# Optimization experiments

Measured on AMD Instinct MI355X. Metric: run time of the kernel, lower is better.

The kernel has to match this reference:

```python
import jax, jax.numpy as jnp
import numpy as np
import math

B, N_SEQ, SEQ_LEN, C_M = 1, 256, 256, 256
N_HEADS, C_HIDDEN = 8, 32
HC = N_HEADS * C_HIDDEN
LN_EPS = 1e-5


def setup_inputs() -> dict:
    key = jax.random.key(0)
    ks = jax.random.split(key, 8)
    s_in = 1.0 / math.sqrt(C_M)
    s_out = 1.0 / math.sqrt(HC)
    return {
        "m": jax.random.normal(ks[0], (B, N_SEQ, SEQ_LEN, C_M), dtype=jnp.float32),
        "ln_w": jnp.ones((C_M,), dtype=jnp.float32),
        "ln_b": jnp.zeros((C_M,), dtype=jnp.float32),
        "wq": jax.random.normal(ks[1], (C_M, HC), dtype=jnp.float32) * s_in,
        "wk": jax.random.normal(ks[2], (C_M, HC), dtype=jnp.float32) * s_in,
        "wv": jax.random.normal(ks[3], (C_M, HC), dtype=jnp.float32) * s_in,
        "wg": jax.random.normal(ks[4], (C_M, HC), dtype=jnp.float32) * s_in,
        "bg": jnp.zeros((HC,), dtype=jnp.float32),
        "wo": jax.random.normal(ks[5], (HC, C_M), dtype=jnp.float32) * s_out,
        "bo": jnp.zeros((C_M,), dtype=jnp.float32),
    }


def reference(m, ln_w, ln_b, wq, wk, wv, wg, bg, wo, bo):
    b, s, l, _ = m.shape  # [B, n_seq, seq_len, c_m]
    # LayerNorm over c_m
    mu = jnp.mean(m, axis=-1, keepdims=True)
    var = jnp.mean(jnp.square(m - mu), axis=-1, keepdims=True)
    mn = (m - mu) * jax.lax.rsqrt(var + LN_EPS) * ln_w + ln_b  # [B, S, L, c_m]
    mt = jnp.swapaxes(mn, 1, 2)  # [B, L, S, c_m] -- attend over n_seq per column
    # QKV projections (no bias), split heads: [B, L, H, S, ch]
    def proj(w):
        return jnp.transpose(
            (mt @ w).reshape(b, l, s, N_HEADS, C_HIDDEN), (0, 1, 3, 2, 4)
        )
    q, k, v = proj(wq), proj(wk), proj(wv)
    logits = jnp.einsum("blhsc,blhtc->blhst", q, k) / math.sqrt(C_HIDDEN)
    weights = jax.nn.softmax(logits, axis=-1)
    o = jnp.einsum("blhst,blhtc->blhsc", weights, v)  # [B, L, H, S, ch]
    # Faithful to source: permute(0,2,1,3,4) -> [B, H, L, S, ch], then raw reshape
    o = jnp.transpose(o, (0, 2, 1, 3, 4))
    o = o.reshape(b, s, l, HC)  # data-scrambling reshape, as in source
    # Sigmoid gating on layer-normed input (m.transpose(1,2).transpose(1,2) == mn)
    g = jax.nn.sigmoid(mn @ wg + bg)  # [B, S, L, HC]
    o = g * o
    return o @ wo + bo  # [B, S, L, c_m]
```

## Files before the change

### kernel.cpp

```cpp
#include <hip/hip_runtime.h>

typedef unsigned short u16;
typedef __attribute__((ext_vector_type(8))) short bf16x8;
typedef __attribute__((ext_vector_type(4))) float f32x4;

__device__ __forceinline__ u16 f2b(float f){
  __bf16 h = (__bf16)f;
  return __builtin_bit_cast(u16, h);
}

__global__ __launch_bounds__(256) void k_pre(const float* __restrict__ m,
    const float* __restrict__ lw, const float* __restrict__ lb,
    const float* __restrict__ wq, const float* __restrict__ wk,
    const float* __restrict__ wv, const float* __restrict__ wg,
    const float* __restrict__ wo,
    u16* __restrict__ mnb, u16* __restrict__ mnb2, u16* __restrict__ WT){
  __shared__ u16 T[16*264];
  int bx = blockIdx.x;
  int tid = threadIdx.x;
  if (bx < 2048){
    int l = bx>>3;
    int s0 = (bx&7)*32 + (tid>>6)*8;
    int ln = tid&63;
    float4 w = *(const float4*)(lw + ln*4);
    float4 b = *(const float4*)(lb + ln*4);
    #pragma unroll
    for (int i=0;i<8;++i){
      int s = s0 + i;
      float4 x = *(const float4*)(m + ((size_t)s*256 + l)*256 + ln*4);
      float s1 = x.x+x.y+x.z+x.w;
      float s2 = x.x*x.x + x.y*x.y + x.z*x.z + x.w*x.w;
      #pragma unroll
      for (int off=32; off>0; off>>=1){
        s1 += __shfl_xor(s1, off);
        s2 += __shfl_xor(s2, off);
      }
      float mu  = s1*(1.0f/256.0f);
      float inv = rsqrtf(s2*(1.0f/256.0f) - mu*mu + 1e-5f);
      u16 o[4];
      o[0] = f2b((x.x-mu)*inv*w.x + b.x);
      o[1] = f2b((x.y-mu)*inv*w.y + b.y);
      o[2] = f2b((x.z-mu)*inv*w.z + b.z);
      o[3] = f2b((x.w-mu)*inv*w.w + b.w);
      *(ushort4*)(mnb  + ((size_t)l*256 + s)*256 + ln*4) = *(ushort4*)o;
      *(ushort4*)(mnb2 + ((size_t)s*256 + l)*256 + ln*4) = *(ushort4*)o;
    }
  } else {
    int bb = bx - 2048;
    int z = bb>>4, n0 = (bb&15)*16;
    const float* W = (z==0)?wq:(z==1)?wk:(z==2)?wv:(z==3)?wg:wo;
    int nl = tid&15;
    #pragma unroll
    for (int i=0;i<16;++i){
      int cm = i*16 + (tid>>4);
      T[nl*264 + cm] = f2b(W[(size_t)cm*256 + n0 + nl]);
    }
    __syncthreads();
    int n = tid>>4, cc = (tid&15)*16;
    uint4 a = *(const uint4*)&T[n*264 + cc];
    uint4 c = *(const uint4*)&T[n*264 + cc + 8];
    *(uint4*)&WT[(size_t)z*65536 + (size_t)(n0+n)*256 + cc]     = a;
    *(uint4*)&WT[(size_t)z*65536 + (size_t)(n0+n)*256 + cc + 8] = c;
  }
}

__global__ __launch_bounds__(256,3) void k_fused(const u16* __restrict__ mnb,
    const u16* __restrict__ mnb2, const u16* __restrict__ WT,
    const float* __restrict__ bg, const float* __restrict__ bo,
    float* __restrict__ outp){
  __shared__ u16 smem[26880];
  u16* QS = smem;
  u16* KS = smem + 10240;
  u16* VT = smem + 18432;
  u16* PB = smem;
  float* OS = (float*)smem;
  u16* GS = smem + 18432;

  int bx = blockIdx.x;
  int l = ((bx&7)<<5) | (bx>>6);
  int h = (bx>>3)&7;
  int tid = threadIdx.x;
  int lane = tid&63, wid = tid>>6, quad = lane>>4, lo = lane&15;
  int m0 = wid*64;
  f32x4 z4 = {0.f,0.f,0.f,0.f};

  const u16* Abase = mnb + (size_t)l*65536;
  const u16* Bq = WT + (size_t)h*32*256;
  const u16* Bk = WT + (size_t)65536 + (size_t)h*32*256;
  const u16* Bv = WT + (size_t)2*65536 + (size_t)h*32*256;
  f32x4 acc[4][6];
  #pragma unroll
  for (int a=0;a<4;++a)
    #pragma unroll
    for (int b=0;b<6;++b) acc[a][b]=z4;

  for (int ks=0; ks<8; ++ks){
    bf16x8 af[4];
    #pragma unroll
    for (int mt=0; mt<4; ++mt)
      af[mt] = *(const bf16x8*)(Abase + (size_t)(m0+mt*16+lo)*256 + ks*32 + quad*8);
    bf16x8 bq[2], bk2[2], bv2[2];
    #pragma unroll
    for (int c2=0; c2<2; ++c2){
      bq[c2]  = *(const bf16x8*)(Bq + (size_t)(c2*16+lo)*256 + ks*32 + quad*8);
      bk2[c2] = *(const bf16x8*)(Bk + (size_t)(c2*16+lo)*256 + ks*32 + quad*8);
      bv2[c2] = *(const bf16x8*)(Bv + (size_t)(c2*16+lo)*256 + ks*32 + quad*8);
    }
    #pragma unroll
    for (int mt=0; mt<4; ++mt){
      #pragma unroll
      for (int c2=0; c2<2; ++c2){
        acc[mt][0+c2] = __builtin_amdgcn_mfma_f32_16x16x32_bf16(af[mt], bq[c2],  acc[mt][0+c2], 0,0,0);
        acc[mt][2+c2] = __builtin_amdgcn_mfma_f32_16x16x32_bf16(af[mt], bk2[c2], acc[mt][2+c2], 0,0,0);
        acc[mt][4+c2] = __builtin_amdgcn_mfma_f32_16x16x32_bf16(af[mt], bv2[c2], acc[mt][4+c2], 0,0,0);
      }
    }
  }
  #pragma unroll
  for (int mt=0; mt<4; ++mt)
    #pragma unroll
    for (int ntl=0; ntl<2; ++ntl)
      #pragma unroll
      for (int r=0; r<4; ++r){
        int s = m0 + mt*16 + quad*4 + r;
        QS[s*40 + ntl*16+lo] = f2b(acc[mt][0+ntl][r]);
        KS[s*32 + ntl*16+lo] = f2b(acc[mt][2+ntl][r]);
        VT[(ntl*16+lo)*264 + s] = f2b(acc[mt][4+ntl][r]);
      }
  bf16x8 qf[4];
  #pragma unroll
  for (int mt=0; mt<4; ++mt)
    qf[mt] = *(const bf16x8*)&QS[(m0+mt*16+lo)*40 + quad*8];
  __syncthreads();

  const float scale = 0.17677669529663687f;
  float lr[16];
  #pragma unroll
  for (int i=0;i<16;++i) lr[i]=0.f;
  f32x4 o_acc[4][2];
  #pragma unroll
  for (int a=0;a<4;++a){ o_acc[a][0]=z4; o_acc[a][1]=z4; }
  int pbase = wid*64*40;

  for (int ts=0; ts<8; ++ts){
    bf16x8 kf[2];
    #pragma unroll
    for (int ntl=0; ntl<2; ++ntl)
      kf[ntl] = *(const bf16x8*)&KS[(ts*32+ntl*16+lo)*32 + quad*8];
    bf16x8 vf[2];
    #pragma unroll
    for (int nc=0; nc<2; ++nc)
      vf[nc] = *(const bf16x8*)&VT[(nc*16+lo)*264 + ts*32 + quad*8];
    #pragma unroll
    for (int mt=0; mt<4; ++mt){
      f32x4 sa[2];
      sa[0] = __builtin_amdgcn_mfma_f32_16x16x32_bf16(qf[mt], kf[0], z4, 0,0,0);
      sa[1] = __builtin_amdgcn_mfma_f32_16x16x32_bf16(qf[mt], kf[1], z4, 0,0,0);
      #pragma unroll
      for (int ntl=0; ntl<2; ++ntl)
        #pragma unroll
        for (int r=0; r<4; ++r){
          float p = __expf(sa[ntl][r]*scale);
          lr[mt*4+r] += p;
          PB[pbase + (mt*16+quad*4+r)*40 + ntl*16+lo] = f2b(p);
        }
      bf16x8 paf = *(const bf16x8*)&PB[pbase + (mt*16+lo)*40 + quad*8];
      o_acc[mt][0] = __builtin_amdgcn_mfma_f32_16x16x32_bf16(paf, vf[0], o_acc[mt][0], 0,0,0);
      o_acc[mt][1] = __builtin_amdgcn_mfma_f32_16x16x32_bf16(paf, vf[1], o_acc[mt][1], 0,0,0);
    }
  }
  #pragma unroll
  for (int i=0;i<16;++i){
    float v = lr[i];
    v += __shfl_xor(v, 1);
    v += __shfl_xor(v, 2);
    v += __shfl_xor(v, 4);
    v += __shfl_xor(v, 8);
    lr[i] = 1.0f / v;
  }
  __syncthreads();
  #pragma unroll
  for (int mt=0; mt<4; ++mt)
    #pragma unroll
    for (int nc=0; nc<2; ++nc)
      #pragma unroll
      for (int r=0; r<4; ++r){
        int s = m0 + mt*16 + quad*4 + r;
        int c = nc*16 + lo;
        OS[s*32 + c] = o_acc[mt][nc][r] * lr[mt*4+r];
      }
  __syncthreads();

  int sp  = h*32 + (l>>3);
  int l0p = (l&7)*32;
  int wn0 = wid*64;
  const u16* Gw = WT + (size_t)3*65536;
  const u16* A2 = mnb2 + (size_t)sp*65536;
  f32x4 gacc[2][4];
  #pragma unroll
  for (int a=0;a<2;++a)
    #pragma unroll
    for (int b=0;b<4;++b) gacc[a][b]=z4;
  for (int ks=0; ks<8; ++ks){
    bf16x8 ga[2];
    #pragma unroll
    for (int mt2=0; mt2<2; ++mt2)
      ga[mt2] = *(const bf16x8*)(A2 + (size_t)(l0p+mt2*16+lo)*256 + ks*32 + quad*8);
    bf16x8 gb[4];
    #pragma unroll
    for (int nt=0; nt<4; ++nt)
      gb[nt] = *(const bf16x8*)(Gw + (size_t)(wn0+nt*16+lo)*256 + ks*32 + quad*8);
    #pragma unroll
    for (int mt2=0; mt2<2; ++mt2)
      #pragma unroll
      for (int nt=0; nt<4; ++nt)
        gacc[mt2][nt] = __builtin_amdgcn_mfma_f32_16x16x32_bf16(ga[mt2], gb[nt], gacc[mt2][nt], 0,0,0);
  }
  #pragma unroll
  for (int nt=0; nt<4; ++nt){
    int n = wn0 + nt*16 + lo;
    float bgn = bg[n];
    #pragma unroll
    for (int mt2=0; mt2<2; ++mt2)
      #pragma unroll
      for (int r=0; r<4; ++r){
        int j = mt2*16 + quad*4 + r;
        float g = 1.f/(1.f + __expf(-(gacc[mt2][nt][r] + bgn)));
        GS[j*264 + n] = f2b(g * OS[j*256 + n]);
      }
  }
  __syncthreads();

  const u16* Ow = WT + (size_t)4*65536;
  f32x4 pacc[2][4];
  #pragma unroll
  for (int a=0;a<2;++a)
    #pragma unroll
    for (int b=0;b<4;++b) pacc[a][b]=z4;
  for (int ks=0; ks<8; ++ks){
    bf16x8 pa[2];
    #pragma unroll
    for (int mt2=0; mt2<2; ++mt2)
      pa[mt2] = *(const bf16x8*)&GS[(mt2*16+lo)*264 + ks*32 + quad*8];
    bf16x8 pb[4];
    #pragma unroll
    for (int nt=0; nt<4; ++nt)
      pb[nt] = *(const bf16x8*)(Ow + (size_t)(wn0+nt*16+lo)*256 + ks*32 + quad*8);
    #pragma unroll
    for (int mt2=0; mt2<2; ++mt2)
      #pragma unroll
      for (int nt=0; nt<4; ++nt)
        pacc[mt2][nt] = __builtin_amdgcn_mfma_f32_16x16x32_bf16(pa[mt2], pb[nt], pacc[mt2][nt], 0,0,0);
  }
  #pragma unroll
  for (int nt=0; nt<4; ++nt){
    int n = wn0 + nt*16 + lo;
    float bon = bo[n];
    #pragma unroll
    for (int mt2=0; mt2<2; ++mt2)
      #pragma unroll
      for (int r=0; r<4; ++r){
        int j = mt2*16 + quad*4 + r;
        outp[((size_t)sp*256 + l0p + j)*256 + n] = pacc[mt2][nt][r] + bon;
      }
  }
}

extern "C" void kernel_launch(void* const* d_in, const int* in_sizes, int n_in,
                              void* d_out, int out_size, void* d_ws, size_t ws_size,
                              hipStream_t stream){
  const float* m  = (const float*)d_in[0];
  const float* lw = (const float*)d_in[1];
  const float* lb = (const float*)d_in[2];
  const float* wq = (const float*)d_in[3];
  const float* wk = (const float*)d_in[4];
  const float* wv = (const float*)d_in[5];
  const float* wg = (const float*)d_in[6];
  const float* bg = (const float*)d_in[7];
  const float* wo = (const float*)d_in[8];
  const float* bo = (const float*)d_in[9];

  u16* mnb  = (u16*)d_ws;
  u16* mnb2 = mnb  + (size_t)16777216;
  u16* WT   = mnb2 + (size_t)16777216;
  float* out = (float*)d_out;

  k_pre  <<<2128, 256, 0, stream>>>(m, lw, lb, wq, wk, wv, wg, wo, mnb, mnb2, WT);
  k_fused<<<2048, 256, 0, stream>>>(mnb, mnb2, WT, bg, bo, out);
}
```

Measured before the change: 308.5 us.

## Drop second normalized copy; gather gate operand via async LDS loads

The pre-kernel no longer writes a second s-major copy of the layer-normed activations. That removes 32 MB of bf16 writes and the later reads of that copy. The fused kernel instead gathers the gate GEMM's A rows from the single l-major copy straight into LDS with global_load_lds, using an XOR swizzle, and issues this at kernel start so it overlaps the QKV projection. Q is staged through a small per-wave scratch, V is stored in a new interleaved layout, and each thread in the LN kernel now handles 8 elements. The gathered loads are strided (512 B chunks, 128 KB apart), which may hurt coalescing, and an extra barrier is added.

Result: faster. 300.4 us (-2.6%).

```diff
diff --git a/kernel.cpp b/kernel.cpp
--- a/kernel.cpp
+++ b/kernel.cpp
@@ -7,6 +7,12 @@
 __device__ __forceinline__ u16 f2b(float f){
   __bf16 h = (__bf16)f;
   return __builtin_bit_cast(u16, h);
+}
+
+__device__ __forceinline__ void gload_lds16(const void* g, void* l){
+  __builtin_amdgcn_global_load_lds(
+      (const __attribute__((address_space(1))) unsigned int*)g,
+      (__attribute__((address_space(3))) unsigned int*)l, 16, 0, 0);
 }
 
 __global__ __launch_bounds__(256) void k_pre(const float* __restrict__ m,
@@ -14,36 +20,44 @@
     const float* __restrict__ wq, const float* __restrict__ wk,
     const float* __restrict__ wv, const float* __restrict__ wg,
     const float* __restrict__ wo,
-    u16* __restrict__ mnb, u16* __restrict__ mnb2, u16* __restrict__ WT){
+    u16* __restrict__ mnb, u16* __restrict__ WT){
   __shared__ u16 T[16*264];
-  int bx = blockIdx.x;
-  int tid = threadIdx.x;
+  int bx = blockIdx.x, tid = threadIdx.x;
   if (bx < 2048){
     int l = bx>>3;
-    int s0 = (bx&7)*32 + (tid>>6)*8;
-    int ln = tid&63;
-    float4 w = *(const float4*)(lw + ln*4);
-    float4 b = *(const float4*)(lb + ln*4);
-    #pragma unroll
-    for (int i=0;i<8;++i){
-      int s = s0 + i;
-      float4 x = *(const float4*)(m + ((size_t)s*256 + l)*256 + ln*4);
-      float s1 = x.x+x.y+x.z+x.w;
-      float s2 = x.x*x.x + x.y*x.y + x.z*x.z + x.w*x.w;
-      #pragma unroll
-      for (int off=32; off>0; off>>=1){
+    int w = tid>>6, ln = tid&63, half = ln>>5, lh = ln&31;
+    float4 wa = *(const float4*)(lw + lh*8);
+    float4 wb = *(const float4*)(lw + lh*8 + 4);
+    float4 ba = *(const float4*)(lb + lh*8);
+    float4 bb = *(const float4*)(lb + lh*8 + 4);
+    #pragma unroll
+    for (int i=0;i<4;++i){
+      int s = (bx&7)*32 + w*8 + i*2 + half;
+      const float* mp = m + ((size_t)s*256 + l)*256 + lh*8;
+      float4 xa = *(const float4*)mp;
+      float4 xb = *(const float4*)(mp+4);
+      float s1 = (xa.x+xa.y)+(xa.z+xa.w) + (xb.x+xb.y)+(xb.z+xb.w);
+      float s2 = xa.x*xa.x+xa.y*xa.y+xa.z*xa.z+xa.w*xa.w
+               + xb.x*xb.x+xb.y*xb.y+xb.z*xb.z+xb.w*xb.w;
+      #pragma unroll
+      for (int off=16; off>0; off>>=1){
         s1 += __shfl_xor(s1, off);
         s2 += __shfl_xor(s2, off);
       }
       float mu  = s1*(1.0f/256.0f);
       float inv = rsqrtf(s2*(1.0f/256.0f) - mu*mu + 1e-5f);
-      u16 o[4];
-      o[0] = f2b((x.x-mu)*inv*w.x + b.x);
-      o[1] = f2b((x.y-mu)*inv*w.y + b.y);
-      o[2] = f2b((x.z-mu)*inv*w.z + b.z);
-      o[3] = f2b((x.w-mu)*inv*w.w + b.w);
-      *(ushort4*)(mnb  + ((size_t)l*256 + s)*256 + ln*4) = *(ushort4*)o;
-      *(ushort4*)(mnb2 + ((size_t)s*256 + l)*256 + ln*4) = *(ushort4*)o;
+      u16 o[8];
+      o[0]=f2b((xa.x-mu)*inv*wa.x+ba.x);
+      o[1]=f2b((xa.y-mu)*inv*wa.y+ba.y);
+      o[2]=f2b((xa.z-mu)*inv*wa.z+ba.z);
+      o[3]=f2b((xa.w-mu)*inv*wa.w+ba.w);
+      o[4]=f2b((xb.x-mu)*inv*wb.x+bb.x);
+      o[5]=f2b((xb.y-mu)*inv*wb.y+bb.y);
+      o[6]=f2b((xb.z-mu)*inv*wb.z+bb.z);
+      o[7]=f2b((xb.w-mu)*inv*wb.w+bb.w);
+      u16* op = mnb + ((size_t)l*256 + s)*256 + lh*8;
+      *(ushort4*)op     = *(ushort4*)&o[0];
+      *(ushort4*)(op+4) = *(ushort4*)&o[4];
     }
   } else {
     int bb = bx - 2048;
@@ -65,16 +79,14 @@
 }
 
 __global__ __launch_bounds__(256,3) void k_fused(const u16* __restrict__ mnb,
-    const u16* __restrict__ mnb2, const u16* __restrict__ WT,
-    const float* __restrict__ bg, const float* __restrict__ bo,
-    float* __restrict__ outp){
-  __shared__ u16 smem[26880];
-  u16* QS = smem;
-  u16* KS = smem + 10240;
-  u16* VT = smem + 18432;
-  u16* PB = smem;
+    const u16* __restrict__ WT, const float* __restrict__ bg,
+    const float* __restrict__ bo, float* __restrict__ outp){
+  __shared__ u16 smem[27136];
+  u16* KS  = smem + 2560;
+  u16* VT2 = smem + 10752;
+  u16* GAB = smem + 18944;
   float* OS = (float*)smem;
-  u16* GS = smem + 18432;
+  u16* GS  = smem + 16384;
 
   int bx = blockIdx.x;
   int l = ((bx&7)<<5) | (bx>>6);
@@ -82,7 +94,22 @@
   int tid = threadIdx.x;
   int lane = tid&63, wid = tid>>6, quad = lane>>4, lo = lane&15;
   int m0 = wid*64;
+  u16* SC = smem + wid*640;
   f32x4 z4 = {0.f,0.f,0.f,0.f};
+  int sp  = h*32 + (l>>3);
+  int l0p = (l&7)*32;
+
+  {
+    const char* mb = (const char*)mnb;
+    #pragma unroll
+    for (int c2=0;c2<4;++c2){
+      int r   = wid*8 + c2*2 + (lane>>5);
+      int dst = (wid*8 + c2*2)*256;
+      size_t src = (size_t)(l0p + r)*131072 + (size_t)sp*512
+                 + (size_t)((((lane&31)*16) ^ ((r&7)<<4)));
+      gload_lds16(mb + src, &GAB[dst]);
+    }
+  }
 
   const u16* Abase = mnb + (size_t)l*65536;
   const u16* Bq = WT + (size_t)h*32*256;
@@ -122,15 +149,21 @@
     for (int ntl=0; ntl<2; ++ntl)
       #pragma unroll
       for (int r=0; r<4; ++r){
-        int s = m0 + mt*16 + quad*4 + r;
-        QS[s*40 + ntl*16+lo] = f2b(acc[mt][0+ntl][r]);
-        KS[s*32 + ntl*16+lo] = f2b(acc[mt][2+ntl][r]);
-        VT[(ntl*16+lo)*264 + s] = f2b(acc[mt][4+ntl][r]);
+        int t = m0 + mt*16 + quad*4 + r;
+        int c = ntl*16 + lo;
+        KS[t*32 + c] = f2b(acc[mt][2+ntl][r]);
+        VT2[(t>>3)*256 + c*8 + (t&7)] = f2b(acc[mt][4+ntl][r]);
       }
   bf16x8 qf[4];
   #pragma unroll
-  for (int mt=0; mt<4; ++mt)
-    qf[mt] = *(const bf16x8*)&QS[(m0+mt*16+lo)*40 + quad*8];
+  for (int mt=0; mt<4; ++mt){
+    #pragma unroll
+    for (int ntl=0; ntl<2; ++ntl)
+      #pragma unroll
+      for (int r=0; r<4; ++r)
+        SC[(quad*4+r)*40 + ntl*16+lo] = f2b(acc[mt][0+ntl][r]);
+    qf[mt] = *(const bf16x8*)&SC[lo*40 + quad*8];
+  }
   __syncthreads();
 
   const float scale = 0.17677669529663687f;
@@ -140,7 +173,6 @@
   f32x4 o_acc[4][2];
   #pragma unroll
   for (int a=0;a<4;++a){ o_acc[a][0]=z4; o_acc[a][1]=z4; }
-  int pbase = wid*64*40;
 
   for (int ts=0; ts<8; ++ts){
     bf16x8 kf[2];
@@ -150,7 +182,7 @@
     bf16x8 vf[2];
     #pragma unroll
     for (int nc=0; nc<2; ++nc)
-      vf[nc] = *(const bf16x8*)&VT[(nc*16+lo)*264 + ts*32 + quad*8];
+      vf[nc] = *(const bf16x8*)&VT2[(ts*4+quad)*256 + (nc*16+lo)*8];
     #pragma unroll
     for (int mt=0; mt<4; ++mt){
       f32x4 sa[2];
@@ -162,9 +194,9 @@
         for (int r=0; r<4; ++r){
           float p = __expf(sa[ntl][r]*scale);
           lr[mt*4+r] += p;
-          PB[pbase + (mt*16+quad*4+r)*40 + ntl*16+lo] = f2b(p);
+          SC[(quad*4+r)*40 + ntl*16+lo] = f2b(p);
         }
-      bf16x8 paf = *(const bf16x8*)&PB[pbase + (mt*16+lo)*40 + quad*8];
+      bf16x8 paf = *(const bf16x8*)&SC[lo*40 + quad*8];
       o_acc[mt][0] = __builtin_amdgcn_mfma_f32_16x16x32_bf16(paf, vf[0], o_acc[mt][0], 0,0,0);
       o_acc[mt][1] = __builtin_amdgcn_mfma_f32_16x16x32_bf16(paf, vf[1], o_acc[mt][1], 0,0,0);
     }
@@ -191,11 +223,8 @@
       }
   __syncthreads();
 
-  int sp  = h*32 + (l>>3);
-  int l0p = (l&7)*32;
   int wn0 = wid*64;
   const u16* Gw = WT + (size_t)3*65536;
-  const u16* A2 = mnb2 + (size_t)sp*65536;
   f32x4 gacc[2][4];
   #pragma unroll
   for (int a=0;a<2;++a)
@@ -204,8 +233,10 @@
   for (int ks=0; ks<8; ++ks){
     bf16x8 ga[2];
     #pragma unroll
-    for (int mt2=0; mt2<2; ++mt2)
-      ga[mt2] = *(const bf16x8*)(A2 + (size_t)(l0p+mt2*16+lo)*256 + ks*32 + quad*8);
+    for (int mt2=0; mt2<2; ++mt2){
+      int j = mt2*16 + lo;
+      ga[mt2] = *(const bf16x8*)&GAB[j*256 + ((ks*32 + quad*8) ^ ((j&7)<<3))];
+    }
     bf16x8 gb[4];
     #pragma unroll
     for (int nt=0; nt<4; ++nt)
@@ -216,6 +247,7 @@
       for (int nt=0; nt<4; ++nt)
         gacc[mt2][nt] = __builtin_amdgcn_mfma_f32_16x16x32_bf16(ga[mt2], gb[nt], gacc[mt2][nt], 0,0,0);
   }
+  __syncthreads();
   #pragma unroll
   for (int nt=0; nt<4; ++nt){
     int n = wn0 + nt*16 + lo;
@@ -280,11 +312,10 @@
   const float* wo = (const float*)d_in[8];
   const float* bo = (const float*)d_in[9];
 
-  u16* mnb  = (u16*)d_ws;
-  u16* mnb2 = mnb  + (size_t)16777216;
-  u16* WT   = mnb2 + (size_t)16777216;
+  u16* mnb = (u16*)d_ws;
+  u16* WT  = mnb + (size_t)16777216;
   float* out = (float*)d_out;
 
-  k_pre  <<<2128, 256, 0, stream>>>(m, lw, lb, wq, wk, wv, wg, wo, mnb, mnb2, WT);
-  k_fused<<<2048, 256, 0, stream>>>(mnb, mnb2, WT, bg, bo, out);
-}
+  k_pre  <<<2128, 256, 0, stream>>>(m, lw, lb, wq, wk, wv, wg, wo, mnb, WT);
+  k_fused<<<2048, 256, 0, stream>>>(mnb, WT, bg, bo, out);
+}
```
